# Performance work log

Measured on AMD Instinct MI355X. Metric: run time of the kernel, lower is better.

The kernel has to match this reference:

```python
import jax, jax.numpy as jnp
import numpy as np

B, N, C = 2, 30, 320
FH = FW = 64          # feature map (latent 128 / downsample 2)
PH = PW = 32          # roi_scale output size at this level
ORIG = 128.0          # original (latent) spatial size
SCALE = 0.5           # spatial_scale = 1/downsample_rate
SR = 2                # sampling_ratio
M = N + 1             # global channel + rois


def _bilinear(img, y, x):
    # img: (C, H, W); y, x: arbitrary-shape float coords. torchvision-style:
    # zero outside [-1, H]/[ -1, W], clamp then 4-corner interp.
    H, W = img.shape[1], img.shape[2]
    valid = (y > -1.0) & (y < H) & (x > -1.0) & (x < W)
    yc = jnp.clip(y, 0.0, H - 1.0)
    xc = jnp.clip(x, 0.0, W - 1.0)
    y0 = jnp.floor(yc).astype(jnp.int32)
    x0 = jnp.floor(xc).astype(jnp.int32)
    y1 = jnp.minimum(y0 + 1, H - 1)
    x1 = jnp.minimum(x0 + 1, W - 1)
    wy = yc - y0
    wx = xc - x0
    v = (img[:, y0, x0] * (1 - wy) * (1 - wx)
         + img[:, y0, x1] * (1 - wy) * wx
         + img[:, y1, x0] * wy * (1 - wx)
         + img[:, y1, x1] * wy * wx)
    return v * valid


def _roi_align_one(img, x1, y1, bw, bh):
    # img (C,FH,FW); x1,y1,bw,bh (N,) in aligned feature coords / bin sizes
    s = (jnp.arange(PH * SR, dtype=img.dtype) + 0.5) / SR   # sub-sample offsets in bin units
    yy = y1[:, None] + s[None, :] * bh[:, None]             # (N, PH*SR)
    xx = x1[:, None] + s[None, :] * bw[:, None]             # (N, PW*SR)
    yg = jnp.broadcast_to(yy[:, :, None], (N, PH * SR, PW * SR))
    xg = jnp.broadcast_to(xx[:, None, :], (N, PH * SR, PW * SR))
    v = _bilinear(img, yg, xg)                              # (C, N, PH*SR, PW*SR)
    v = v.reshape(C, N, PH, SR, PW, SR).mean(axis=(3, 5))   # average sub-samples
    return v.transpose(1, 0, 2, 3)                          # (N, C, PH, PW)


def _roi_unpool_one(roi_imgs, x1, y1, bw, bh):
    # inverse of roi_align: paste each (C,PH,PW) roi back into its own (FH,FW) map
    ys = jnp.arange(FH, dtype=roi_imgs.dtype)
    xs = jnp.arange(FW, dtype=roi_imgs.dtype)
    ry = (ys[None, :] - y1[:, None]) / bh[:, None] - 0.5    # (N, FH) roi-grid coords
    rx = (xs[None, :] - x1[:, None]) / bw[:, None] - 0.5    # (N, FW)
    ryg = jnp.broadcast_to(ry[:, :, None], (N, FH, FW))
    rxg = jnp.broadcast_to(rx[:, None, :], (N, FH, FW))
    return jax.vmap(_bilinear)(roi_imgs, ryg, rxg)          # (N, C, FH, FW); zeros outside box


def _fuser(x, perm, w_reduce, w1, b1, w2, b2):
    # FuseWeightGenerator: x (B, M, C, H, W)
    fg = jnp.sum(x, axis=2) != 0                            # (B, M, H, W) foreground mask
    fw = jnp.einsum('bmchw,c->bmhw', x, w_reduce)           # 1x1 conv C->1, no bias
    g = fw[:, :1]
    r = fw[:, 1:][:, perm]                                  # shuffle roi channels
    gin = jnp.concatenate([g, r], axis=1)                   # (B, M, H, W)
    # ChannelGate: only the 'max' branch affects the output (original uses last channel_att_raw)
    mp = gin.max(axis=(2, 3))                               # (B, M)
    att = jax.nn.relu(mp @ w1 + b1) @ w2 + b2
    gated = gin * jax.nn.sigmoid(att)[:, :, None, None]
    inv = jnp.argsort(perm)
    fw = jnp.concatenate([gated[:, :1], gated[:, 1:][:, inv]], axis=1)
    fw = jnp.where(fg, fw, jnp.finfo(fw.dtype).min)
    w = jax.nn.softmax(fw, axis=1)[:, :, None]              # (B, M, 1, H, W)
    return jnp.sum(x * w, axis=1)                           # (B, C, H, W)


def _forward(normed_hidden_states, attn_output, instance_boxes, instance_masks, perm,
             w_reduce, w1, b1, w2, b2):
    fmap = normed_hidden_states.reshape(B, FH, FW, C).transpose(0, 3, 1, 2)  # b c h w
    boxes = instance_boxes * ORIG * SCALE - 0.5             # aligned=True feature coords
    x1, y1 = boxes[..., 0], boxes[..., 1]
    x2, y2 = boxes[..., 2], boxes[..., 3]
    bw = (x2 - x1) / PW
    bh = (y2 - y1) / PH
    roi_feats = jax.vmap(_roi_align_one)(fmap, x1, y1, bw, bh)   # (B,N,C,PH,PW)
    mask = instance_masks.astype(roi_feats.dtype)[:, :, None, None, None]
    roi_feats = roi_feats * mask                             # masked rois stay zero
    unpooled = jax.vmap(_roi_unpool_one)(roi_feats, x1, y1, bw, bh) * mask  # (B,N,C,FH,FW)
    attn_map = attn_output.reshape(B, FH, FW, C).transpose(0, 3, 1, 2)[:, None]
    x = jnp.concatenate([attn_map, unpooled], axis=1)        # (B, M, C, FH, FW)
    fused = _fuser(x, perm, w_reduce, w1, b1, w2, b2)        # (B, C, FH, FW)
    return fused.transpose(0, 2, 3, 1).reshape(B, FH * FW, C)


def setup_inputs() -> dict:
    key = jax.random.key(0)
    ks = jax.random.split(key, 10)
    nhs = jax.random.normal(ks[0], (B, FH * FW, C), dtype=jnp.float32)
    attn = jax.random.normal(ks[1], (B, FH * FW, C), dtype=jnp.float32)
    cx = jax.random.uniform(ks[2], (B, N), minval=0.25, maxval=0.75)
    cy = jax.random.uniform(ks[3], (B, N), minval=0.25, maxval=0.75)
    hw = jax.random.uniform(ks[4], (B, N, 2), minval=0.1, maxval=0.4)
    boxes = jnp.stack([cx - hw[..., 0] / 2, cy - hw[..., 1] / 2,
                       cx + hw[..., 0] / 2, cy + hw[..., 1] / 2], axis=-1)
    boxes = jnp.clip(boxes, 0.0, 1.0).astype(jnp.float32)    # normalized xyxy
    masks = jax.random.randint(ks[5], (B, N), 0, 2).astype(jnp.int32)
    perm = jax.random.permutation(ks[6], N).astype(jnp.int32)
    w_reduce = (jax.random.normal(ks[7], (C,), dtype=jnp.float32) / np.sqrt(C)).astype(jnp.float32)
    w1 = (jax.random.normal(ks[8], (M, M), dtype=jnp.float32) / np.sqrt(M)).astype(jnp.float32)
    b1 = jnp.zeros((M,), dtype=jnp.float32)
    w2 = (jax.random.normal(ks[9], (M, M), dtype=jnp.float32) / np.sqrt(M)).astype(jnp.float32)
    b2 = jnp.zeros((M,), dtype=jnp.float32)
    return {"normed_hidden_states": nhs, "attn_output": attn, "instance_boxes": boxes,
            "instance_masks": masks, "perm": perm, "w_reduce": w_reduce,
            "w1": w1, "b1": b1, "w2": w2, "b2": b2}


def reference(normed_hidden_states, attn_output, instance_boxes, instance_masks, perm,
              w_reduce, w1, b1, w2, b2):
    return _forward(normed_hidden_states, attn_output, instance_boxes, instance_masks, perm,
                    w_reduce, w1, b1, w2, b2)
```

## Files before the change

kernel.cpp:

```cpp
#include <hip/hip_runtime.h>
#include <hip/hip_bf16.h>

#define NB 2
#define NN 30
#define NC 320
#define NM 31
#define HW 4096
#define FMIN_F (-3.40282346638528859812e+38f)
#define PCH 8

typedef float nfloat4 __attribute__((ext_vector_type(4)));

#define OFF_FSUM   0
#define OFF_FWRED  8192
#define OFF_ASUM   16384
#define OFF_AWRED  24576
#define OFF_Z      32768
#define OFF_MP     286720
#define WS_FLOATS  286784

#define GRID_ROIF (NB * NN * 128)
#define GRID_RED  1639

__device__ __forceinline__ void get_box(const float* boxes, int b, int n,
                                        float& x1, float& y1, float& bw, float& bh) {
    const float* p = boxes + (b * NN + n) * 4;
    float X1 = p[0] * 64.0f - 0.5f;
    float Y1 = p[1] * 64.0f - 0.5f;
    float X2 = p[2] * 64.0f - 0.5f;
    float Y2 = p[3] * 64.0f - 0.5f;
    x1 = X1; y1 = Y1;
    bw = (X2 - X1) / 32.0f;
    bh = (Y2 - Y1) / 32.0f;
}

__device__ __forceinline__ unsigned short f2bf(float f) {
    __hip_bfloat16 h = __float2bfloat16(f);
    return *reinterpret_cast<unsigned short*>(&h);
}
__device__ __forceinline__ unsigned pack2(float a, float b) {
    return (unsigned)f2bf(a) | ((unsigned)f2bf(b) << 16);
}
__device__ __forceinline__ float blo(unsigned u) { return __uint_as_float(u << 16); }
__device__ __forceinline__ float bhi(unsigned u) { return __uint_as_float(u & 0xffff0000u); }

__device__ __forceinline__ unsigned encf(float f) {
    unsigned u = __float_as_uint(f);
    return (u & 0x80000000u) ? ~u : (u | 0x80000000u);
}
__device__ __forceinline__ float decf(unsigned e) {
    unsigned u = (e & 0x80000000u) ? (e & 0x7fffffffu) : ~e;
    return __uint_as_float(u);
}

__device__ void do_roifeat(int blk, const float* __restrict__ nhs,
                           const float* __restrict__ boxes,
                           const int* __restrict__ masks,
                           unsigned* __restrict__ roif) {
    int bn = blk >> 7;
    int n = bn % NN;
    int b = bn / NN;
    if (masks[b * NN + n] == 0) return;
    __shared__ float wsm[8][9];
    __shared__ int bsm[8];
    int tid = threadIdx.x;
    float x1, y1, bw, bh;
    get_box(boxes, b, n, x1, y1, bw, bh);

    if (tid < 8) {
        int cell = blk * 8 + tid;
        int q = cell & 31;
        int p = (cell >> 5) & 31;
        float W[9] = {0.f,0.f,0.f,0.f,0.f,0.f,0.f,0.f,0.f};
        float wys[4], wxs[4];
        int iy0s[4], ix0s[4];
        int iymin = 64, ixmin = 64;
#pragma unroll
        for (int s_ = 0; s_ < 4; s_++) {
            int di = s_ >> 1, dj = s_ & 1;
            float y = y1 + ((float)p + 0.25f + 0.5f * (float)di) * bh;
            float x = x1 + ((float)q + 0.25f + 0.5f * (float)dj) * bw;
            float yc = fminf(fmaxf(y, 0.0f), 63.0f);
            float xc = fminf(fmaxf(x, 0.0f), 63.0f);
            int iy0 = (int)floorf(yc), ix0 = (int)floorf(xc);
            wys[s_] = yc - (float)iy0;
            wxs[s_] = xc - (float)ix0;
            iy0s[s_] = iy0; ix0s[s_] = ix0;
            iymin = min(iymin, iy0); ixmin = min(ixmin, ix0);
        }
#pragma unroll
        for (int s_ = 0; s_ < 4; s_++) {
            float wy = wys[s_], wx = wxs[s_];
            int dy = iy0s[s_] - iymin;
            int dx = ix0s[s_] - ixmin;
            bool yt = (iy0s[s_] == 63);
            bool xt = (ix0s[s_] == 63);
            float ay0 = yt ? 1.0f : (1.0f - wy);
            float ay1 = yt ? 0.0f : wy;
            float ax0 = xt ? 1.0f : (1.0f - wx);
            float ax1 = xt ? 0.0f : wx;
            float r0 = dy ? 0.0f : ay0;
            float r1 = dy ? ay0  : ay1;
            float r2 = dy ? ay1  : 0.0f;
            float c0 = dx ? 0.0f : ax0;
            float c1 = dx ? ax0  : ax1;
            float c2 = dx ? ax1  : 0.0f;
            W[0] += r0 * c0; W[1] += r0 * c1; W[2] += r0 * c2;
            W[3] += r1 * c0; W[4] += r1 * c1; W[5] += r1 * c2;
            W[6] += r2 * c0; W[7] += r2 * c1; W[8] += r2 * c2;
        }
#pragma unroll
        for (int k = 0; k < 9; k++) wsm[tid][k] = W[k] * 0.25f;
        bsm[tid] = iymin * 64 + ixmin;
    }
    __syncthreads();

    int cid = tid / 40;
    int v = tid - cid * 40;
    int cell = blk * 8 + cid;
    const float4* fb4 = (const float4*)(nhs + (size_t)b * HW * NC);
    int base = bsm[cid];
    float4 acc0 = make_float4(0.f, 0.f, 0.f, 0.f);
    float4 acc1 = make_float4(0.f, 0.f, 0.f, 0.f);
#pragma unroll
    for (int i = 0; i < 3; i++) {
#pragma unroll
        for (int j = 0; j < 3; j++) {
            float w = wsm[cid][i * 3 + j];
            if (w != 0.0f) {
                int off = (base + i * 64 + j) * 80 + v * 2;
                float4 f0 = fb4[off];
                float4 f1 = fb4[off + 1];
                acc0.x += w * f0.x; acc0.y += w * f0.y;
                acc0.z += w * f0.z; acc0.w += w * f0.w;
                acc1.x += w * f1.x; acc1.y += w * f1.y;
                acc1.z += w * f1.z; acc1.w += w * f1.w;
            }
        }
    }
    uint4 pk;
    pk.x = pack2(acc0.x, acc0.y);
    pk.y = pack2(acc0.z, acc0.w);
    pk.z = pack2(acc1.x, acc1.y);
    pk.w = pack2(acc1.z, acc1.w);
    ((uint4*)roif)[(size_t)cell * 40 + v] = pk;
}

__device__ void do_reduce(int rblk, const float* __restrict__ nhs,
                          const float* __restrict__ attn,
                          const float* __restrict__ wred, float* __restrict__ ws) {
    if (rblk == 0 && threadIdx.x < 64)
        ((unsigned*)(ws + OFF_MP))[threadIdx.x] = 0u;
    int wave = threadIdx.x >> 6;
    int lane = threadIdx.x & 63;
    int row = rblk * 5 + wave;
    if (row >= NB * HW) return;
    const float4* n4 = (const float4*)(nhs + (size_t)row * NC);
    const float4* a4 = (const float4*)(attn + (size_t)row * NC);
    const float4* w4 = (const float4*)wred;
    float4 wv = w4[lane];
    float4 nv = n4[lane];
    float4 av = a4[lane];
    float s_n = nv.x + nv.y + nv.z + nv.w;
    float w_n = nv.x * wv.x + nv.y * wv.y + nv.z * wv.z + nv.w * wv.w;
    float s_a = av.x + av.y + av.z + av.w;
    float w_a = av.x * wv.x + av.y * wv.y + av.z * wv.z + av.w * wv.w;
    if (lane < 16) {
        float4 wv2 = w4[lane + 64];
        float4 nv2 = n4[lane + 64];
        float4 av2 = a4[lane + 64];
        s_n += nv2.x + nv2.y + nv2.z + nv2.w;
        w_n += nv2.x * wv2.x + nv2.y * wv2.y + nv2.z * wv2.z + nv2.w * wv2.w;
        s_a += av2.x + av2.y + av2.z + av2.w;
        w_a += av2.x * wv2.x + av2.y * wv2.y + av2.z * wv2.z + av2.w * wv2.w;
    }
#pragma unroll
    for (int off = 32; off > 0; off >>= 1) {
        s_n += __shfl_down(s_n, off, 64);
        w_n += __shfl_down(w_n, off, 64);
        s_a += __shfl_down(s_a, off, 64);
        w_a += __shfl_down(w_a, off, 64);
    }
    if (lane == 0) {
        ws[OFF_FSUM + row]  = s_n;
        ws[OFF_FWRED + row] = w_n;
        ws[OFF_ASUM + row]  = s_a;
        ws[OFF_AWRED + row] = w_a;
    }
}

__global__ void k_stage1(const float* __restrict__ nhs, const float* __restrict__ attn,
                         const float* __restrict__ boxes, const int* __restrict__ masks,
                         const float* __restrict__ wred, float* __restrict__ ws,
                         unsigned* __restrict__ roif) {
    int blk = blockIdx.x;
    if (blk < GRID_ROIF) {
        do_roifeat(blk, nhs, boxes, masks, roif);
    } else {
        do_reduce(blk - GRID_ROIF, nhs, attn, wred, ws);
    }
}

__global__ void k_fw(const float* __restrict__ boxes, const int* __restrict__ masks,
                     float* __restrict__ ws) {
    int bm = blockIdx.x / PCH;
    int ch = blockIdx.x % PCH;
    int b = bm / NM, m = bm % NM;
    int pix0 = ch * (HW / PCH);
    __shared__ float rs[1024], rw[1024];
    __shared__ float red[256];
    float locmax = -INFINITY;
    int tid = threadIdx.x;
    if (m == 0) {
        for (int pix = pix0 + tid; pix < pix0 + HW / PCH; pix += 256) {
            float fwv = ws[OFF_AWRED + b * HW + pix];
            bool fg = (ws[OFF_ASUM + b * HW + pix] != 0.0f);
            ws[OFF_Z + (size_t)bm * HW + pix] = fg ? fwv : FMIN_F;
            locmax = fmaxf(locmax, fwv);
        }
    } else {
        int n = m - 1;
        int msk = masks[b * NN + n];
        if (msk) {
            float x1, y1, bw, bh;
            get_box(boxes, b, n, x1, y1, bw, bh);
            int h0 = pix0 >> 6;
            float ry_lo = ((float)h0 - y1) / bh - 0.5f;
            float ry_hi = ((float)(h0 + 7) - y1) / bh - 0.5f;
            int iy_lo = max(0, (int)floorf(fminf(fmaxf(ry_lo, 0.0f), 31.0f)) - 1);
            int iy_hi = min(31, (int)floorf(fminf(fmaxf(ry_hi, 0.0f), 31.0f)) + 2);
            const float* fsum  = ws + OFF_FSUM + b * HW;
            const float* fwred = ws + OFF_FWRED + b * HW;
            for (int cell = tid; cell < 1024; cell += 256) {
                int q = cell & 31, p = cell >> 5;
                if (p < iy_lo || p > iy_hi) continue;
                float accs = 0.f, accw = 0.f;
#pragma unroll
                for (int di = 0; di < 2; di++) {
#pragma unroll
                    for (int dj = 0; dj < 2; dj++) {
                        float y = y1 + ((float)p + 0.25f + 0.5f * (float)di) * bh;
                        float x = x1 + ((float)q + 0.25f + 0.5f * (float)dj) * bw;
                        float yc = fminf(fmaxf(y, 0.0f), 63.0f);
                        float xc = fminf(fmaxf(x, 0.0f), 63.0f);
                        int iy0 = (int)floorf(yc), ix0 = (int)floorf(xc);
                        int iy1 = min(iy0 + 1, 63), ix1 = min(ix0 + 1, 63);
                        float wy = yc - (float)iy0, wx = xc - (float)ix0;
                        float w00 = (1.f - wy) * (1.f - wx), w01 = (1.f - wy) * wx;
                        float w10 = wy * (1.f - wx), w11 = wy * wx;
                        accs += w00 * fsum[iy0 * 64 + ix0] + w01 * fsum[iy0 * 64 + ix1]
                              + w10 * fsum[iy1 * 64 + ix0] + w11 * fsum[iy1 * 64 + ix1];
                        accw += w00 * fwred[iy0 * 64 + ix0] + w01 * fwred[iy0 * 64 + ix1]
                              + w10 * fwred[iy1 * 64 + ix0] + w11 * fwred[iy1 * 64 + ix1];
                    }
                }
                rs[cell] = accs * 0.25f;
                rw[cell] = accw * 0.25f;
            }
            __syncthreads();
            for (int pix = pix0 + tid; pix < pix0 + HW / PCH; pix += 256) {
                int h = pix >> 6, wp = pix & 63;
                float fwv = 0.0f;
                bool fg = false;
                float ry = ((float)h - y1) / bh - 0.5f;
                float rx = ((float)wp - x1) / bw - 0.5f;
                bool valid = (ry > -1.0f) && (ry < 32.0f) && (rx > -1.0f) && (rx < 32.0f);
                if (valid) {
                    float yc = fminf(fmaxf(ry, 0.0f), 31.0f);
                    float xc = fminf(fmaxf(rx, 0.0f), 31.0f);
                    int iy0 = (int)floorf(yc), ix0 = (int)floorf(xc);
                    int iy1 = min(iy0 + 1, 31), ix1 = min(ix0 + 1, 31);
                    float wy = yc - (float)iy0, wx = xc - (float)ix0;
                    float w00 = (1.f - wy) * (1.f - wx), w01 = (1.f - wy) * wx;
                    float w10 = wy * (1.f - wx), w11 = wy * wx;
                    fwv = w00 * rw[iy0 * 32 + ix0] + w01 * rw[iy0 * 32 + ix1]
                        + w10 * rw[iy1 * 32 + ix0] + w11 * rw[iy1 * 32 + ix1];
                    float su = w00 * rs[iy0 * 32 + ix0] + w01 * rs[iy0 * 32 + ix1]
                             + w10 * rs[iy1 * 32 + ix0] + w11 * rs[iy1 * 32 + ix1];
                    fg = (su != 0.0f);
                }
                ws[OFF_Z + (size_t)bm * HW + pix] = fg ? fwv : FMIN_F;
                locmax = fmaxf(locmax, fwv);
            }
        } else {
            for (int pix = pix0 + tid; pix < pix0 + HW / PCH; pix += 256)
                ws[OFF_Z + (size_t)bm * HW + pix] = FMIN_F;
            locmax = 0.0f;
        }
    }
    red[tid] = locmax;
    __syncthreads();
    for (int s = 128; s > 0; s >>= 1) {
        if (tid < s) red[tid] = fmaxf(red[tid], red[tid + s]);
        __syncthreads();
    }
    if (tid == 0)
        atomicMax((unsigned*)(ws + OFF_MP) + bm, encf(red[0]));
}

__global__ void k_final(const float* __restrict__ attn, const float* __restrict__ boxes,
                        const int* __restrict__ perm, const float* __restrict__ w1,
                        const float* __restrict__ b1, const float* __restrict__ w2,
                        const float* __restrict__ b2, const float* __restrict__ ws,
                        const unsigned* __restrict__ roif, float* __restrict__ out) {
    __shared__ float mpg[NM], hb[NM], scal[32], wbuf[8][32];
    __shared__ int acnt[8];
    __shared__ unsigned char alist[8][NN];
    int t = threadIdx.x;
    int idx0 = blockIdx.x * 8;
    int b = idx0 >> 12;

    if (t < 8) acnt[t] = 0;
    if (t < NM) {
        unsigned e = ((const unsigned*)(ws + OFF_MP))[b * NM + ((t == 0) ? 0 : 1 + perm[t - 1])];
        mpg[t] = decf(e);
    }
    __syncthreads();
    if (t < NM) {
        float a = b1[t];
#pragma unroll
        for (int k = 0; k < NM; k++) a += mpg[k] * w1[k * NM + t];
        hb[t] = fmaxf(a, 0.0f);
    }
    __syncthreads();
    if (t < NM) {
        float a = b2[t];
#pragma unroll
        for (int k = 0; k < NM; k++) a += hb[k] * w2[k * NM + t];
        float sig = 1.0f / (1.0f + expf(-a));
        if (t == 0) scal[0] = sig;
        else        scal[1 + perm[t - 1]] = sig;
    }
    __syncthreads();

    if (t < 256) {
        int pg = t >> 5, m = t & 31;
        int pix = (idx0 + pg) & 4095;
        float zz = FMIN_F;
        if (m < NM) {
            float v = ws[OFF_Z + (size_t)(b * NM + m) * HW + pix];
            zz = (v == FMIN_F) ? FMIN_F : v * scal[m];
        }
        float mx = zz;
#pragma unroll
        for (int off = 16; off > 0; off >>= 1)
            mx = fmaxf(mx, __shfl_xor(mx, off, 64));
        float e = (m < NM) ? expf(zz - mx) : 0.0f;
        float s = e;
#pragma unroll
        for (int off = 16; off > 0; off >>= 1)
            s += __shfl_xor(s, off, 64);
        if (m < NM) {
            float w = e / s;
            wbuf[pg][m] = w;
            if (m >= 1 && w != 0.0f) {
                int pos = atomicAdd(&acnt[pg], 1);
                alist[pg][pos] = (unsigned char)(m - 1);
            }
        }
    }
    __syncthreads();

    int pid = t / 40;
    int v = t - pid * 40;
    int idx = idx0 + pid;
    int pix = idx & 4095;
    int h = pix >> 6, wp = pix & 63;
    float w0 = wbuf[pid][0];
    const float4* at4 = (const float4*)attn;
    float4 a0 = at4[(size_t)idx * 80 + v * 2];
    float4 a1 = at4[(size_t)idx * 80 + v * 2 + 1];
    float4 acc0, acc1;
    acc0.x = a0.x * w0; acc0.y = a0.y * w0; acc0.z = a0.z * w0; acc0.w = a0.w * w0;
    acc1.x = a1.x * w0; acc1.y = a1.y * w0; acc1.z = a1.z * w0; acc1.w = a1.w * w0;
    const uint4* r4 = (const uint4*)roif;
    int na = acnt[pid];
    for (int k = 0; k < na; k++) {
        int n = alist[pid][k];
        float wn = wbuf[pid][n + 1];
        float x1, y1, bw, bh;
        get_box(boxes, b, n, x1, y1, bw, bh);
        float ry = ((float)h - y1) / bh - 0.5f;
        float rx = ((float)wp - x1) / bw - 0.5f;
        float yc = fminf(fmaxf(ry, 0.0f), 31.0f);
        float xc = fminf(fmaxf(rx, 0.0f), 31.0f);
        int iy0 = (int)floorf(yc), ix0 = (int)floorf(xc);
        int iy1 = min(iy0 + 1, 31), ix1 = min(ix0 + 1, 31);
        float wy = yc - (float)iy0, wx = xc - (float)ix0;
        float w00 = (1.f - wy) * (1.f - wx) * wn, w01 = (1.f - wy) * wx * wn;
        float w10 = wy * (1.f - wx) * wn, w11 = wy * wx * wn;
        size_t base = ((size_t)(b * NN + n)) << 10;
        uint4 U00 = r4[(base + iy0 * 32 + ix0) * 40 + v];
        uint4 U01 = r4[(base + iy0 * 32 + ix1) * 40 + v];
        uint4 U10 = r4[(base + iy1 * 32 + ix0) * 40 + v];
        uint4 U11 = r4[(base + iy1 * 32 + ix1) * 40 + v];
        acc0.x += w00 * blo(U00.x) + w01 * blo(U01.x) + w10 * blo(U10.x) + w11 * blo(U11.x);
        acc0.y += w00 * bhi(U00.x) + w01 * bhi(U01.x) + w10 * bhi(U10.x) + w11 * bhi(U11.x);
        acc0.z += w00 * blo(U00.y) + w01 * blo(U01.y) + w10 * blo(U10.y) + w11 * blo(U11.y);
        acc0.w += w00 * bhi(U00.y) + w01 * bhi(U01.y) + w10 * bhi(U10.y) + w11 * bhi(U11.y);
        acc1.x += w00 * blo(U00.z) + w01 * blo(U01.z) + w10 * blo(U10.z) + w11 * blo(U11.z);
        acc1.y += w00 * bhi(U00.z) + w01 * bhi(U01.z) + w10 * bhi(U10.z) + w11 * bhi(U11.z);
        acc1.z += w00 * blo(U00.w) + w01 * blo(U01.w) + w10 * blo(U10.w) + w11 * blo(U11.w);
        acc1.w += w00 * bhi(U00.w) + w01 * bhi(U01.w) + w10 * bhi(U10.w) + w11 * bhi(U11.w);
    }
    nfloat4 nv0 = { acc0.x, acc0.y, acc0.z, acc0.w };
    nfloat4 nv1 = { acc1.x, acc1.y, acc1.z, acc1.w };
    __builtin_nontemporal_store(nv0, ((nfloat4*)out) + (size_t)idx * 80 + v * 2);
    __builtin_nontemporal_store(nv1, ((nfloat4*)out) + (size_t)idx * 80 + v * 2 + 1);
}

extern "C" void kernel_launch(void* const* d_in, const int* in_sizes, int n_in,
                              void* d_out, int out_size, void* d_ws, size_t ws_size,
                              hipStream_t stream) {
    const float* nhs   = (const float*)d_in[0];
    const float* attn  = (const float*)d_in[1];
    const float* boxes = (const float*)d_in[2];
    const int*   masks = (const int*)d_in[3];
    const int*   perm  = (const int*)d_in[4];
    const float* wred  = (const float*)d_in[5];
    const float* w1    = (const float*)d_in[6];
    const float* b1    = (const float*)d_in[7];
    const float* w2    = (const float*)d_in[8];
    const float* b2    = (const float*)d_in[9];
    float* out = (float*)d_out;
    float* ws = (float*)d_ws;
    unsigned* roif = (unsigned*)((char*)d_ws + (size_t)WS_FLOATS * 4);

    k_stage1<<<GRID_ROIF + GRID_RED, 320, 0, stream>>>(nhs, attn, boxes, masks, wred, ws, roif);
    k_fw<<<NB * NM * PCH, 256, 0, stream>>>(boxes, masks, ws);
    k_final<<<NB * HW / 8, 320, 0, stream>>>(attn, boxes, perm, w1, b1, w2, b2, ws, roif, out);
}
```

Measured before the change: 117.4 us.

## Pre-convert features to bf16 and merge roi-align with foreground-weight stage

The row-reduction pass now also writes a bf16 copy of the hidden states. The roi-align gather then reads that half-size copy instead of the fp32 features. The roi-align blocks are fused with the foreground-weight blocks into one launch, and the block max-reduction now uses wave shuffles. This is meant to cut gather bandwidth and remove one kernel boundary, at the cost of an extra 10 MB write in the first pass and bf16 rounding of the inputs to roi-align.

```diff
diff --git a/kernel.cpp b/kernel.cpp
--- a/kernel.cpp
+++ b/kernel.cpp
@@ -18,8 +18,11 @@
 #define OFF_Z      32768
 #define OFF_MP     286720
 #define WS_FLOATS  286784
+#define ROIF_BYTE  1147136
+#define NHSBF_BYTE (ROIF_BYTE + 39321600)
 
 #define GRID_ROIF (NB * NN * 128)
+#define GRID_FW   (NB * NM * PCH)
 #define GRID_RED  1639
 
 __device__ __forceinline__ void get_box(const float* boxes, int b, int n,
@@ -53,16 +56,62 @@
     return __uint_as_float(u);
 }
 
-__device__ void do_roifeat(int blk, const float* __restrict__ nhs,
+__global__ void k_pre(const float* __restrict__ nhs, const float* __restrict__ attn,
+                      const float* __restrict__ wred, float* __restrict__ ws,
+                      unsigned* __restrict__ nbf) {
+    if (blockIdx.x == 0 && threadIdx.x < 64)
+        ((unsigned*)(ws + OFF_MP))[threadIdx.x] = 0u;
+    int wave = threadIdx.x >> 6;
+    int lane = threadIdx.x & 63;
+    int row = blockIdx.x * 5 + wave;
+    if (row >= NB * HW) return;
+    const float4* n4 = (const float4*)(nhs + (size_t)row * NC);
+    const float4* a4 = (const float4*)(attn + (size_t)row * NC);
+    const float4* w4 = (const float4*)wred;
+    float4 wv = w4[lane];
+    float4 nv = n4[lane];
+    float4 av = a4[lane];
+    uint2 pk0; pk0.x = pack2(nv.x, nv.y); pk0.y = pack2(nv.z, nv.w);
+    ((uint2*)nbf)[(size_t)row * 80 + lane] = pk0;
+    float s_n = nv.x + nv.y + nv.z + nv.w;
+    float w_n = nv.x * wv.x + nv.y * wv.y + nv.z * wv.z + nv.w * wv.w;
+    float s_a = av.x + av.y + av.z + av.w;
+    float w_a = av.x * wv.x + av.y * wv.y + av.z * wv.z + av.w * wv.w;
+    if (lane < 16) {
+        float4 wv2 = w4[lane + 64];
+        float4 nv2 = n4[lane + 64];
+        float4 av2 = a4[lane + 64];
+        uint2 pk1; pk1.x = pack2(nv2.x, nv2.y); pk1.y = pack2(nv2.z, nv2.w);
+        ((uint2*)nbf)[(size_t)row * 80 + 64 + lane] = pk1;
+        s_n += nv2.x + nv2.y + nv2.z + nv2.w;
+        w_n += nv2.x * wv2.x + nv2.y * wv2.y + nv2.z * wv2.z + nv2.w * wv2.w;
+        s_a += av2.x + av2.y + av2.z + av2.w;
+        w_a += av2.x * wv2.x + av2.y * wv2.y + av2.z * wv2.z + av2.w * wv2.w;
+    }
+#pragma unroll
+    for (int off = 32; off > 0; off >>= 1) {
+        s_n += __shfl_down(s_n, off, 64);
+        w_n += __shfl_down(w_n, off, 64);
+        s_a += __shfl_down(s_a, off, 64);
+        w_a += __shfl_down(w_a, off, 64);
+    }
+    if (lane == 0) {
+        ws[OFF_FSUM + row]  = s_n;
+        ws[OFF_FWRED + row] = w_n;
+        ws[OFF_ASUM + row]  = s_a;
+        ws[OFF_AWRED + row] = w_a;
+    }
+}
+
+__device__ void do_roifeat(int blk, const unsigned* __restrict__ nbf,
                            const float* __restrict__ boxes,
                            const int* __restrict__ masks,
-                           unsigned* __restrict__ roif) {
+                           unsigned* __restrict__ roif,
+                           float* wsm , int* bsm ) {
     int bn = blk >> 7;
     int n = bn % NN;
     int b = bn / NN;
     if (masks[b * NN + n] == 0) return;
-    __shared__ float wsm[8][9];
-    __shared__ int bsm[8];
     int tid = threadIdx.x;
     float x1, y1, bw, bh;
     get_box(boxes, b, n, x1, y1, bw, bh);
@@ -110,7 +159,7 @@
             W[6] += r2 * c0; W[7] += r2 * c1; W[8] += r2 * c2;
         }
 #pragma unroll
-        for (int k = 0; k < 9; k++) wsm[tid][k] = W[k] * 0.25f;
+        for (int k = 0; k < 9; k++) wsm[tid * 9 + k] = W[k] * 0.25f;
         bsm[tid] = iymin * 64 + ixmin;
     }
     __syncthreads();
@@ -118,7 +167,8 @@
     int cid = tid / 40;
     int v = tid - cid * 40;
     int cell = blk * 8 + cid;
-    const float4* fb4 = (const float4*)(nhs + (size_t)b * HW * NC);
+    const uint4* fb = (const uint4*)nbf;
+    size_t brow = (size_t)b * HW;
     int base = bsm[cid];
     float4 acc0 = make_float4(0.f, 0.f, 0.f, 0.f);
     float4 acc1 = make_float4(0.f, 0.f, 0.f, 0.f);
@@ -126,15 +176,13 @@
     for (int i = 0; i < 3; i++) {
 #pragma unroll
         for (int j = 0; j < 3; j++) {
-            float w = wsm[cid][i * 3 + j];
+            float w = wsm[cid * 9 + i * 3 + j];
             if (w != 0.0f) {
-                int off = (base + i * 64 + j) * 80 + v * 2;
-                float4 f0 = fb4[off];
-                float4 f1 = fb4[off + 1];
-                acc0.x += w * f0.x; acc0.y += w * f0.y;
-                acc0.z += w * f0.z; acc0.w += w * f0.w;
-                acc1.x += w * f1.x; acc1.y += w * f1.y;
-                acc1.z += w * f1.z; acc1.w += w * f1.w;
+                uint4 U = fb[(brow + base + i * 64 + j) * 40 + v];
+                acc0.x += w * blo(U.x); acc0.y += w * bhi(U.x);
+                acc0.z += w * blo(U.y); acc0.w += w * bhi(U.y);
+                acc1.x += w * blo(U.z); acc1.y += w * bhi(U.z);
+                acc1.z += w * blo(U.w); acc1.w += w * bhi(U.w);
             }
         }
     }
@@ -146,73 +194,17 @@
     ((uint4*)roif)[(size_t)cell * 40 + v] = pk;
 }
 
-__device__ void do_reduce(int rblk, const float* __restrict__ nhs,
-                          const float* __restrict__ attn,
-                          const float* __restrict__ wred, float* __restrict__ ws) {
-    if (rblk == 0 && threadIdx.x < 64)
-        ((unsigned*)(ws + OFF_MP))[threadIdx.x] = 0u;
-    int wave = threadIdx.x >> 6;
-    int lane = threadIdx.x & 63;
-    int row = rblk * 5 + wave;
-    if (row >= NB * HW) return;
-    const float4* n4 = (const float4*)(nhs + (size_t)row * NC);
-    const float4* a4 = (const float4*)(attn + (size_t)row * NC);
-    const float4* w4 = (const float4*)wred;
-    float4 wv = w4[lane];
-    float4 nv = n4[lane];
-    float4 av = a4[lane];
-    float s_n = nv.x + nv.y + nv.z + nv.w;
-    float w_n = nv.x * wv.x + nv.y * wv.y + nv.z * wv.z + nv.w * wv.w;
-    float s_a = av.x + av.y + av.z + av.w;
-    float w_a = av.x * wv.x + av.y * wv.y + av.z * wv.z + av.w * wv.w;
-    if (lane < 16) {
-        float4 wv2 = w4[lane + 64];
-        float4 nv2 = n4[lane + 64];
-        float4 av2 = a4[lane + 64];
-        s_n += nv2.x + nv2.y + nv2.z + nv2.w;
-        w_n += nv2.x * wv2.x + nv2.y * wv2.y + nv2.z * wv2.z + nv2.w * wv2.w;
-        s_a += av2.x + av2.y + av2.z + av2.w;
-        w_a += av2.x * wv2.x + av2.y * wv2.y + av2.z * wv2.z + av2.w * wv2.w;
-    }
-#pragma unroll
-    for (int off = 32; off > 0; off >>= 1) {
-        s_n += __shfl_down(s_n, off, 64);
-        w_n += __shfl_down(w_n, off, 64);
-        s_a += __shfl_down(s_a, off, 64);
-        w_a += __shfl_down(w_a, off, 64);
-    }
-    if (lane == 0) {
-        ws[OFF_FSUM + row]  = s_n;
-        ws[OFF_FWRED + row] = w_n;
-        ws[OFF_ASUM + row]  = s_a;
-        ws[OFF_AWRED + row] = w_a;
-    }
-}
-
-__global__ void k_stage1(const float* __restrict__ nhs, const float* __restrict__ attn,
-                         const float* __restrict__ boxes, const int* __restrict__ masks,
-                         const float* __restrict__ wred, float* __restrict__ ws,
-                         unsigned* __restrict__ roif) {
-    int blk = blockIdx.x;
-    if (blk < GRID_ROIF) {
-        do_roifeat(blk, nhs, boxes, masks, roif);
-    } else {
-        do_reduce(blk - GRID_ROIF, nhs, attn, wred, ws);
-    }
-}
-
-__global__ void k_fw(const float* __restrict__ boxes, const int* __restrict__ masks,
-                     float* __restrict__ ws) {
-    int bm = blockIdx.x / PCH;
-    int ch = blockIdx.x % PCH;
+__device__ void do_fw(int unit, const float* __restrict__ boxes,
+                      const int* __restrict__ masks, float* __restrict__ ws,
+                      float* rs , float* rw , float* red ) {
+    int bm = unit / PCH;
+    int ch = unit % PCH;
     int b = bm / NM, m = bm % NM;
     int pix0 = ch * (HW / PCH);
-    __shared__ float rs[1024], rw[1024];
-    __shared__ float red[256];
     float locmax = -INFINITY;
     int tid = threadIdx.x;
     if (m == 0) {
-        for (int pix = pix0 + tid; pix < pix0 + HW / PCH; pix += 256) {
+        for (int pix = pix0 + tid; pix < pix0 + HW / PCH; pix += 320) {
             float fwv = ws[OFF_AWRED + b * HW + pix];
             bool fg = (ws[OFF_ASUM + b * HW + pix] != 0.0f);
             ws[OFF_Z + (size_t)bm * HW + pix] = fg ? fwv : FMIN_F;
@@ -231,7 +223,7 @@
             int iy_hi = min(31, (int)floorf(fminf(fmaxf(ry_hi, 0.0f), 31.0f)) + 2);
             const float* fsum  = ws + OFF_FSUM + b * HW;
             const float* fwred = ws + OFF_FWRED + b * HW;
-            for (int cell = tid; cell < 1024; cell += 256) {
+            for (int cell = tid; cell < 1024; cell += 320) {
                 int q = cell & 31, p = cell >> 5;
                 if (p < iy_lo || p > iy_hi) continue;
                 float accs = 0.f, accw = 0.f;
@@ -258,7 +250,7 @@
                 rw[cell] = accw * 0.25f;
             }
             __syncthreads();
-            for (int pix = pix0 + tid; pix < pix0 + HW / PCH; pix += 256) {
+            for (int pix = pix0 + tid; pix < pix0 + HW / PCH; pix += 320) {
                 int h = pix >> 6, wp = pix & 63;
                 float fwv = 0.0f;
                 bool fg = false;
@@ -283,19 +275,37 @@
                 locmax = fmaxf(locmax, fwv);
             }
         } else {
-            for (int pix = pix0 + tid; pix < pix0 + HW / PCH; pix += 256)
+            for (int pix = pix0 + tid; pix < pix0 + HW / PCH; pix += 320)
                 ws[OFF_Z + (size_t)bm * HW + pix] = FMIN_F;
             locmax = 0.0f;
         }
     }
-    red[tid] = locmax;
-    __syncthreads();
-    for (int s = 128; s > 0; s >>= 1) {
-        if (tid < s) red[tid] = fmaxf(red[tid], red[tid + s]);
-        __syncthreads();
-    }
-    if (tid == 0)
-        atomicMax((unsigned*)(ws + OFF_MP) + bm, encf(red[0]));
+#pragma unroll
+    for (int off = 32; off > 0; off >>= 1)
+        locmax = fmaxf(locmax, __shfl_down(locmax, off, 64));
+    int wid = tid >> 6, lane = tid & 63;
+    if (lane == 0) red[wid] = locmax;
+    __syncthreads();
+    if (tid == 0) {
+        float mx = red[0];
+#pragma unroll
+        for (int k = 1; k < 5; k++) mx = fmaxf(mx, red[k]);
+        atomicMax((unsigned*)(ws + OFF_MP) + bm, encf(mx));
+    }
+}
+
+__global__ void k_stage2(const unsigned* __restrict__ nbf, const float* __restrict__ boxes,
+                         const int* __restrict__ masks, float* __restrict__ ws,
+                         unsigned* __restrict__ roif) {
+    __shared__ float smem[2048 + 80];
+    __shared__ int bsm[8];
+    __shared__ float red[5];
+    int blk = blockIdx.x;
+    if (blk < GRID_ROIF) {
+        do_roifeat(blk, nbf, boxes, masks, roif, smem, bsm);
+    } else {
+        do_fw(blk - GRID_ROIF, boxes, masks, ws, smem, smem + 1024, red);
+    }
 }
 
 __global__ void k_final(const float* __restrict__ attn, const float* __restrict__ boxes,
@@ -424,9 +434,10 @@
     const float* b2    = (const float*)d_in[9];
     float* out = (float*)d_out;
     float* ws = (float*)d_ws;
-    unsigned* roif = (unsigned*)((char*)d_ws + (size_t)WS_FLOATS * 4);
-
-    k_stage1<<<GRID_ROIF + GRID_RED, 320, 0, stream>>>(nhs, attn, boxes, masks, wred, ws, roif);
-    k_fw<<<NB * NM * PCH, 256, 0, stream>>>(boxes, masks, ws);
+    unsigned* roif = (unsigned*)((char*)d_ws + ROIF_BYTE);
+    unsigned* nbf  = (unsigned*)((char*)d_ws + NHSBF_BYTE);
+
+    k_pre<<<GRID_RED, 320, 0, stream>>>(nhs, attn, wred, ws, nbf);
+    k_stage2<<<GRID_ROIF + GRID_FW, 320, 0, stream>>>(nbf, boxes, masks, ws, roif);
     k_final<<<NB * HW / 8, 320, 0, stream>>>(attn, boxes, perm, w1, b1, w2, b2, ws, roif, out);
 }
```

Result: no change. 119.7 us (+1.9%).

## Derive ROI channel sums from pooled features and drop the Z buffer

Applied to the files above, without the earlier changes.

The roi-feature blocks now reduce their pooled 320-channel features into per-cell sum and weighted sums, written straight to the workspace. This removes the separate full nhs read in the reduce blocks and the bilinear resampling of per-pixel reductions in the middle kernel. The middle kernel now only computes per-map maxima, and the final kernel recomputes the unpooled logits on the fly instead of reading a stored Z map. The trade is an extra shared-memory reduction in each roi block and more per-thread arithmetic and scattered loads in the final kernel.

```diff
diff --git a/kernel.cpp b/kernel.cpp
--- a/kernel.cpp
+++ b/kernel.cpp
@@ -7,17 +7,17 @@
 #define NM 31
 #define HW 4096
 #define FMIN_F (-3.40282346638528859812e+38f)
-#define PCH 8
+#define FCH 4
 
 typedef float nfloat4 __attribute__((ext_vector_type(4)));
 
-#define OFF_FSUM   0
-#define OFF_FWRED  8192
-#define OFF_ASUM   16384
-#define OFF_AWRED  24576
-#define OFF_Z      32768
-#define OFF_MP     286720
-#define WS_FLOATS  286784
+#define OFF_ASUM   0
+#define OFF_AWRED  8192
+#define OFF_RS     16384
+#define OFF_RW     77824
+#define OFF_MP     139264
+#define WS_FLOATS  139328
+#define ROIF_BYTE  557312
 
 #define GRID_ROIF (NB * NN * 128)
 #define GRID_RED  1639
@@ -56,13 +56,15 @@
 __device__ void do_roifeat(int blk, const float* __restrict__ nhs,
                            const float* __restrict__ boxes,
                            const int* __restrict__ masks,
-                           unsigned* __restrict__ roif) {
+                           const float* __restrict__ wred,
+                           float* __restrict__ ws,
+                           unsigned* __restrict__ roif,
+                           float* wsm , int* bsm ,
+                           float* partS , float* partW ) {
     int bn = blk >> 7;
     int n = bn % NN;
     int b = bn / NN;
     if (masks[b * NN + n] == 0) return;
-    __shared__ float wsm[8][9];
-    __shared__ int bsm[8];
     int tid = threadIdx.x;
     float x1, y1, bw, bh;
     get_box(boxes, b, n, x1, y1, bw, bh);
@@ -110,7 +112,7 @@
             W[6] += r2 * c0; W[7] += r2 * c1; W[8] += r2 * c2;
         }
 #pragma unroll
-        for (int k = 0; k < 9; k++) wsm[tid][k] = W[k] * 0.25f;
+        for (int k = 0; k < 9; k++) wsm[tid * 9 + k] = W[k] * 0.25f;
         bsm[tid] = iymin * 64 + ixmin;
     }
     __syncthreads();
@@ -126,7 +128,7 @@
     for (int i = 0; i < 3; i++) {
 #pragma unroll
         for (int j = 0; j < 3; j++) {
-            float w = wsm[cid][i * 3 + j];
+            float w = wsm[cid * 9 + i * 3 + j];
             if (w != 0.0f) {
                 int off = (base + i * 64 + j) * 80 + v * 2;
                 float4 f0 = fb4[off];
@@ -144,10 +146,28 @@
     pk.z = pack2(acc1.x, acc1.y);
     pk.w = pack2(acc1.z, acc1.w);
     ((uint4*)roif)[(size_t)cell * 40 + v] = pk;
-}
-
-__device__ void do_reduce(int rblk, const float* __restrict__ nhs,
-                          const float* __restrict__ attn,
+
+    const float4* w4 = (const float4*)wred;
+    float4 wv0 = w4[v * 2];
+    float4 wv1 = w4[v * 2 + 1];
+    partS[tid] = acc0.x + acc0.y + acc0.z + acc0.w + acc1.x + acc1.y + acc1.z + acc1.w;
+    partW[tid] = acc0.x * wv0.x + acc0.y * wv0.y + acc0.z * wv0.z + acc0.w * wv0.w
+               + acc1.x * wv1.x + acc1.y * wv1.y + acc1.z * wv1.z + acc1.w * wv1.w;
+    __syncthreads();
+    if (tid < 8) {
+        float ss = 0.f, ww = 0.f;
+#pragma unroll 8
+        for (int k = 0; k < 40; k++) {
+            ss += partS[tid * 40 + k];
+            ww += partW[tid * 40 + k];
+        }
+        int c2 = blk * 8 + tid;
+        ws[OFF_RS + c2] = ss;
+        ws[OFF_RW + c2] = ww;
+    }
+}
+
+__device__ void do_reduce(int rblk, const float* __restrict__ attn,
                           const float* __restrict__ wred, float* __restrict__ ws) {
     if (rblk == 0 && threadIdx.x < 64)
         ((unsigned*)(ws + OFF_MP))[threadIdx.x] = 0u;
@@ -155,35 +175,24 @@
     int lane = threadIdx.x & 63;
     int row = rblk * 5 + wave;
     if (row >= NB * HW) return;
-    const float4* n4 = (const float4*)(nhs + (size_t)row * NC);
     const float4* a4 = (const float4*)(attn + (size_t)row * NC);
     const float4* w4 = (const float4*)wred;
     float4 wv = w4[lane];
-    float4 nv = n4[lane];
     float4 av = a4[lane];
-    float s_n = nv.x + nv.y + nv.z + nv.w;
-    float w_n = nv.x * wv.x + nv.y * wv.y + nv.z * wv.z + nv.w * wv.w;
     float s_a = av.x + av.y + av.z + av.w;
     float w_a = av.x * wv.x + av.y * wv.y + av.z * wv.z + av.w * wv.w;
     if (lane < 16) {
         float4 wv2 = w4[lane + 64];
-        float4 nv2 = n4[lane + 64];
         float4 av2 = a4[lane + 64];
-        s_n += nv2.x + nv2.y + nv2.z + nv2.w;
-        w_n += nv2.x * wv2.x + nv2.y * wv2.y + nv2.z * wv2.z + nv2.w * wv2.w;
         s_a += av2.x + av2.y + av2.z + av2.w;
         w_a += av2.x * wv2.x + av2.y * wv2.y + av2.z * wv2.z + av2.w * wv2.w;
     }
 #pragma unroll
     for (int off = 32; off > 0; off >>= 1) {
-        s_n += __shfl_down(s_n, off, 64);
-        w_n += __shfl_down(w_n, off, 64);
         s_a += __shfl_down(s_a, off, 64);
         w_a += __shfl_down(w_a, off, 64);
     }
     if (lane == 0) {
-        ws[OFF_FSUM + row]  = s_n;
-        ws[OFF_FWRED + row] = w_n;
         ws[OFF_ASUM + row]  = s_a;
         ws[OFF_AWRED + row] = w_a;
     }
@@ -193,75 +202,120 @@
                          const float* __restrict__ boxes, const int* __restrict__ masks,
                          const float* __restrict__ wred, float* __restrict__ ws,
                          unsigned* __restrict__ roif) {
+    __shared__ float wsm[72];
+    __shared__ int bsm[8];
+    __shared__ float partS[320], partW[320];
     int blk = blockIdx.x;
     if (blk < GRID_ROIF) {
-        do_roifeat(blk, nhs, boxes, masks, roif);
+        do_roifeat(blk, nhs, boxes, masks, wred, ws, roif, wsm, bsm, partS, partW);
     } else {
-        do_reduce(blk - GRID_ROIF, nhs, attn, wred, ws);
-    }
-}
-
-__global__ void k_fw(const float* __restrict__ boxes, const int* __restrict__ masks,
-                     float* __restrict__ ws) {
-    int bm = blockIdx.x / PCH;
-    int ch = blockIdx.x % PCH;
+        do_reduce(blk - GRID_ROIF, attn, wred, ws);
+    }
+}
+
+__global__ void k_fwmax(const float* __restrict__ boxes, const int* __restrict__ masks,
+                        float* __restrict__ ws) {
+    int unit = blockIdx.x;
+    int bm = unit / FCH, ch = unit % FCH;
     int b = bm / NM, m = bm % NM;
-    int pix0 = ch * (HW / PCH);
-    __shared__ float rs[1024], rw[1024];
-    __shared__ float red[256];
+    int pix0 = ch * (HW / FCH);
+    int tid = threadIdx.x;
     float locmax = -INFINITY;
-    int tid = threadIdx.x;
     if (m == 0) {
-        for (int pix = pix0 + tid; pix < pix0 + HW / PCH; pix += 256) {
+        for (int pix = pix0 + tid; pix < pix0 + HW / FCH; pix += 256)
+            locmax = fmaxf(locmax, ws[OFF_AWRED + b * HW + pix]);
+    } else {
+        int n = m - 1;
+        if (masks[b * NN + n]) {
+            float x1, y1, bw, bh;
+            get_box(boxes, b, n, x1, y1, bw, bh);
+            const float* rw = ws + OFF_RW + (b * NN + n) * 1024;
+            for (int pix = pix0 + tid; pix < pix0 + HW / FCH; pix += 256) {
+                int h = pix >> 6, wp = pix & 63;
+                float fwv = 0.0f;
+                float ry = ((float)h - y1) / bh - 0.5f;
+                float rx = ((float)wp - x1) / bw - 0.5f;
+                bool valid = (ry > -1.0f) && (ry < 32.0f) && (rx > -1.0f) && (rx < 32.0f);
+                if (valid) {
+                    float yc = fminf(fmaxf(ry, 0.0f), 31.0f);
+                    float xc = fminf(fmaxf(rx, 0.0f), 31.0f);
+                    int iy0 = (int)floorf(yc), ix0 = (int)floorf(xc);
+                    int iy1 = min(iy0 + 1, 31), ix1 = min(ix0 + 1, 31);
+                    float wy = yc - (float)iy0, wx = xc - (float)ix0;
+                    fwv = (1.f - wy) * (1.f - wx) * rw[iy0 * 32 + ix0]
+                        + (1.f - wy) * wx * rw[iy0 * 32 + ix1]
+                        + wy * (1.f - wx) * rw[iy1 * 32 + ix0]
+                        + wy * wx * rw[iy1 * 32 + ix1];
+                }
+                locmax = fmaxf(locmax, fwv);
+            }
+        } else {
+            locmax = 0.0f;
+        }
+    }
+#pragma unroll
+    for (int off = 32; off > 0; off >>= 1)
+        locmax = fmaxf(locmax, __shfl_down(locmax, off, 64));
+    __shared__ float red[4];
+    int wid = tid >> 6, lane = tid & 63;
+    if (lane == 0) red[wid] = locmax;
+    __syncthreads();
+    if (tid == 0) {
+        float mx = fmaxf(fmaxf(red[0], red[1]), fmaxf(red[2], red[3]));
+        atomicMax((unsigned*)(ws + OFF_MP) + bm, encf(mx));
+    }
+}
+
+__global__ void k_final(const float* __restrict__ attn, const float* __restrict__ boxes,
+                        const int* __restrict__ masks, const int* __restrict__ perm,
+                        const float* __restrict__ w1, const float* __restrict__ b1,
+                        const float* __restrict__ w2, const float* __restrict__ b2,
+                        const float* __restrict__ ws, const unsigned* __restrict__ roif,
+                        float* __restrict__ out) {
+    __shared__ float mpg[NM], hb[NM], scal[32], wbuf[8][32];
+    __shared__ int acnt[8];
+    __shared__ unsigned char alist[8][NN];
+    int t = threadIdx.x;
+    int idx0 = blockIdx.x * 8;
+    int b = idx0 >> 12;
+
+    if (t < 8) acnt[t] = 0;
+    if (t < NM) {
+        unsigned e = ((const unsigned*)(ws + OFF_MP))[b * NM + ((t == 0) ? 0 : 1 + perm[t - 1])];
+        mpg[t] = decf(e);
+    }
+    __syncthreads();
+    if (t < NM) {
+        float a = b1[t];
+#pragma unroll
+        for (int k = 0; k < NM; k++) a += mpg[k] * w1[k * NM + t];
+        hb[t] = fmaxf(a, 0.0f);
+    }
+    __syncthreads();
+    if (t < NM) {
+        float a = b2[t];
+#pragma unroll
+        for (int k = 0; k < NM; k++) a += hb[k] * w2[k * NM + t];
+        float sig = 1.0f / (1.0f + expf(-a));
+        if (t == 0) scal[0] = sig;
+        else        scal[1 + perm[t - 1]] = sig;
+    }
+    __syncthreads();
+
+    if (t < 256) {
+        int pg = t >> 5, m = t & 31;
+        int pix = (idx0 + pg) & 4095;
+        float zz = FMIN_F;
+        if (m == 0) {
             float fwv = ws[OFF_AWRED + b * HW + pix];
             bool fg = (ws[OFF_ASUM + b * HW + pix] != 0.0f);
-            ws[OFF_Z + (size_t)bm * HW + pix] = fg ? fwv : FMIN_F;
-            locmax = fmaxf(locmax, fwv);
-        }
-    } else {
-        int n = m - 1;
-        int msk = masks[b * NN + n];
-        if (msk) {
-            float x1, y1, bw, bh;
-            get_box(boxes, b, n, x1, y1, bw, bh);
-            int h0 = pix0 >> 6;
-            float ry_lo = ((float)h0 - y1) / bh - 0.5f;
-            float ry_hi = ((float)(h0 + 7) - y1) / bh - 0.5f;
-            int iy_lo = max(0, (int)floorf(fminf(fmaxf(ry_lo, 0.0f), 31.0f)) - 1);
-            int iy_hi = min(31, (int)floorf(fminf(fmaxf(ry_hi, 0.0f), 31.0f)) + 2);
-            const float* fsum  = ws + OFF_FSUM + b * HW;
-            const float* fwred = ws + OFF_FWRED + b * HW;
-            for (int cell = tid; cell < 1024; cell += 256) {
-                int q = cell & 31, p = cell >> 5;
-                if (p < iy_lo || p > iy_hi) continue;
-                float accs = 0.f, accw = 0.f;
-#pragma unroll
-                for (int di = 0; di < 2; di++) {
-#pragma unroll
-                    for (int dj = 0; dj < 2; dj++) {
-                        float y = y1 + ((float)p + 0.25f + 0.5f * (float)di) * bh;
-                        float x = x1 + ((float)q + 0.25f + 0.5f * (float)dj) * bw;
-                        float yc = fminf(fmaxf(y, 0.0f), 63.0f);
-                        float xc = fminf(fmaxf(x, 0.0f), 63.0f);
-                        int iy0 = (int)floorf(yc), ix0 = (int)floorf(xc);
-                        int iy1 = min(iy0 + 1, 63), ix1 = min(ix0 + 1, 63);
-                        float wy = yc - (float)iy0, wx = xc - (float)ix0;
-                        float w00 = (1.f - wy) * (1.f - wx), w01 = (1.f - wy) * wx;
-                        float w10 = wy * (1.f - wx), w11 = wy * wx;
-                        accs += w00 * fsum[iy0 * 64 + ix0] + w01 * fsum[iy0 * 64 + ix1]
-                              + w10 * fsum[iy1 * 64 + ix0] + w11 * fsum[iy1 * 64 + ix1];
-                        accw += w00 * fwred[iy0 * 64 + ix0] + w01 * fwred[iy0 * 64 + ix1]
-                              + w10 * fwred[iy1 * 64 + ix0] + w11 * fwred[iy1 * 64 + ix1];
-                    }
-                }
-                rs[cell] = accs * 0.25f;
-                rw[cell] = accw * 0.25f;
-            }
-            __syncthreads();
-            for (int pix = pix0 + tid; pix < pix0 + HW / PCH; pix += 256) {
+            zz = fg ? fwv * scal[0] : FMIN_F;
+        } else if (m < NM) {
+            int n = m - 1;
+            if (masks[b * NN + n]) {
+                float x1, y1, bw, bh;
+                get_box(boxes, b, n, x1, y1, bw, bh);
                 int h = pix >> 6, wp = pix & 63;
-                float fwv = 0.0f;
-                bool fg = false;
                 float ry = ((float)h - y1) / bh - 0.5f;
                 float rx = ((float)wp - x1) / bw - 0.5f;
                 bool valid = (ry > -1.0f) && (ry < 32.0f) && (rx > -1.0f) && (rx < 32.0f);
@@ -273,73 +327,15 @@
                     float wy = yc - (float)iy0, wx = xc - (float)ix0;
                     float w00 = (1.f - wy) * (1.f - wx), w01 = (1.f - wy) * wx;
                     float w10 = wy * (1.f - wx), w11 = wy * wx;
-                    fwv = w00 * rw[iy0 * 32 + ix0] + w01 * rw[iy0 * 32 + ix1]
-                        + w10 * rw[iy1 * 32 + ix0] + w11 * rw[iy1 * 32 + ix1];
-                    float su = w00 * rs[iy0 * 32 + ix0] + w01 * rs[iy0 * 32 + ix1]
-                             + w10 * rs[iy1 * 32 + ix0] + w11 * rs[iy1 * 32 + ix1];
-                    fg = (su != 0.0f);
+                    const float* rw = ws + OFF_RW + (b * NN + n) * 1024;
+                    const float* rs = ws + OFF_RS + (b * NN + n) * 1024;
+                    float fwv = w00 * rw[iy0 * 32 + ix0] + w01 * rw[iy0 * 32 + ix1]
+                              + w10 * rw[iy1 * 32 + ix0] + w11 * rw[iy1 * 32 + ix1];
+                    float su  = w00 * rs[iy0 * 32 + ix0] + w01 * rs[iy0 * 32 + ix1]
+                              + w10 * rs[iy1 * 32 + ix0] + w11 * rs[iy1 * 32 + ix1];
+                    if (su != 0.0f) zz = fwv * scal[m];
                 }
-                ws[OFF_Z + (size_t)bm * HW + pix] = fg ? fwv : FMIN_F;
-                locmax = fmaxf(locmax, fwv);
             }
-        } else {
-            for (int pix = pix0 + tid; pix < pix0 + HW / PCH; pix += 256)
-                ws[OFF_Z + (size_t)bm * HW + pix] = FMIN_F;
-            locmax = 0.0f;
-        }
-    }
-    red[tid] = locmax;
-    __syncthreads();
-    for (int s = 128; s > 0; s >>= 1) {
-        if (tid < s) red[tid] = fmaxf(red[tid], red[tid + s]);
-        __syncthreads();
-    }
-    if (tid == 0)
-        atomicMax((unsigned*)(ws + OFF_MP) + bm, encf(red[0]));
-}
-
-__global__ void k_final(const float* __restrict__ attn, const float* __restrict__ boxes,
-                        const int* __restrict__ perm, const float* __restrict__ w1,
-                        const float* __restrict__ b1, const float* __restrict__ w2,
-                        const float* __restrict__ b2, const float* __restrict__ ws,
-                        const unsigned* __restrict__ roif, float* __restrict__ out) {
-    __shared__ float mpg[NM], hb[NM], scal[32], wbuf[8][32];
-    __shared__ int acnt[8];
-    __shared__ unsigned char alist[8][NN];
-    int t = threadIdx.x;
-    int idx0 = blockIdx.x * 8;
-    int b = idx0 >> 12;
-
-    if (t < 8) acnt[t] = 0;
-    if (t < NM) {
-        unsigned e = ((const unsigned*)(ws + OFF_MP))[b * NM + ((t == 0) ? 0 : 1 + perm[t - 1])];
-        mpg[t] = decf(e);
-    }
-    __syncthreads();
-    if (t < NM) {
-        float a = b1[t];
-#pragma unroll
-        for (int k = 0; k < NM; k++) a += mpg[k] * w1[k * NM + t];
-        hb[t] = fmaxf(a, 0.0f);
-    }
-    __syncthreads();
-    if (t < NM) {
-        float a = b2[t];
-#pragma unroll
-        for (int k = 0; k < NM; k++) a += hb[k] * w2[k * NM + t];
-        float sig = 1.0f / (1.0f + expf(-a));
-        if (t == 0) scal[0] = sig;
-        else        scal[1 + perm[t - 1]] = sig;
-    }
-    __syncthreads();
-
-    if (t < 256) {
-        int pg = t >> 5, m = t & 31;
-        int pix = (idx0 + pg) & 4095;
-        float zz = FMIN_F;
-        if (m < NM) {
-            float v = ws[OFF_Z + (size_t)(b * NM + m) * HW + pix];
-            zz = (v == FMIN_F) ? FMIN_F : v * scal[m];
         }
         float mx = zz;
 #pragma unroll
@@ -424,9 +420,9 @@
     const float* b2    = (const float*)d_in[9];
     float* out = (float*)d_out;
     float* ws = (float*)d_ws;
-    unsigned* roif = (unsigned*)((char*)d_ws + (size_t)WS_FLOATS * 4);
+    unsigned* roif = (unsigned*)((char*)d_ws + ROIF_BYTE);
 
     k_stage1<<<GRID_ROIF + GRID_RED, 320, 0, stream>>>(nhs, attn, boxes, masks, wred, ws, roif);
-    k_fw<<<NB * NM * PCH, 256, 0, stream>>>(boxes, masks, ws);
-    k_final<<<NB * HW / 8, 320, 0, stream>>>(attn, boxes, perm, w1, b1, w2, b2, ws, roif, out);
-}
+    k_fwmax<<<NB * NM * FCH, 256, 0, stream>>>(boxes, masks, ws);
+    k_final<<<NB * HW / 8, 320, 0, stream>>>(attn, boxes, masks, perm, w1, b1, w2, b2, ws, roif, out);
+}
```

Measured after the change: 116.3 us. About the same (-1.0%).
